# Kernel tuning notes

Measured on AMD Instinct MI355X. Metric: run time of the kernel, lower is better.

## Reference

```python
import jax, jax.numpy as jnp
import numpy as np

B, T, D = 8, 512, 512
MAX_DUR = 15          # durations drawn from [0,16) then clamped to >=1
MAX_LEN = T * MAX_DUR # static padded frame length (torch pads to per-batch max)


def setup_inputs() -> dict:
    key = jax.random.key(0)
    kf, kd = jax.random.split(key)
    features = jax.random.normal(kf, (B, T, D), dtype=jnp.float32)
    durations = jax.random.randint(kd, (B, T), 0, 16, dtype=jnp.int32)
    return {"features": features, "durations": durations}


def reference(features, durations):
    """Duration-based length regulation (variable-length expand + pad).

    For each batch b, phoneme t is repeated durations[b,t] times along the
    frame axis; sequences are zero-padded to MAX_LEN. Implemented as a
    vectorized cumsum + searchsorted gather (no per-element host syncs).
    """
    Bv, Tv, Dv = features.shape
    dur = jnp.maximum(durations, 1)               # clamp(min=1) as in forward()
    cum = jnp.cumsum(dur, axis=1)                 # (B, T) exclusive-right frame boundaries
    pos = jnp.arange(MAX_LEN, dtype=cum.dtype)    # (MAX_LEN,)
    # idx[b, n] = source phoneme for output frame n: count of boundaries <= n
    idx = jax.vmap(lambda c: jnp.searchsorted(c, pos, side="right"))(cum)  # (B, MAX_LEN)
    valid = pos[None, :] < cum[:, -1:]            # (B, MAX_LEN) frames within total length
    idx = jnp.minimum(idx, Tv - 1)                # keep gather in-bounds for padded frames
    out = jnp.take_along_axis(features, idx[..., None], axis=1)  # (B, MAX_LEN, D)
    return jnp.where(valid[..., None], out, jnp.zeros((), features.dtype))
```

## Files before the change

kernel.cpp:

```cpp
#include <hip/hip_runtime.h>

#define BB 8
#define TT 512
#define DD 512
#define MAX_LEN 7680
#define FPB 30
#define HPB (FPB / 2)
#define BPB (MAX_LEN / FPB)

__global__ __launch_bounds__(256) void regulate_kernel(
    const float4* __restrict__ feat,
    const int2*   __restrict__ dur2,
    float4*       __restrict__ out)
{
    __shared__ int ps[256];
    __shared__ int idx_s[FPB];

    const int t    = threadIdx.x;
    const int b    = blockIdx.x / BPB;
    const int base = (blockIdx.x % BPB) * FPB;

    int2 dd = dur2[b * (TT / 2) + t];
    int d0 = dd.x < 1 ? 1 : dd.x;
    int d1 = dd.y < 1 ? 1 : dd.y;
    ps[t] = d0 + d1;

    if (t < FPB) idx_s[t] = -1;
    __syncthreads();

#pragma unroll
    for (int off = 1; off < 256; off <<= 1) {
        int x = (t >= off) ? ps[t - off] : 0;
        __syncthreads();
        ps[t] += x;
        __syncthreads();
    }
    const int incl = ps[t];
    const int s1   = incl - d1;
    const int s0   = s1 - d0;

    const int lim = base + FPB;
    {
        int k0 = s0 > base ? s0 : base;
        int k1 = s1 < lim  ? s1 : lim;
        for (int k = k0; k < k1; ++k) idx_s[k - base] = 2 * t;
        int k2 = s1 > base ? s1 : base;
        int k3 = incl < lim ? incl : lim;
        for (int k = k2; k < k3; ++k) idx_s[k - base] = 2 * t + 1;
    }
    __syncthreads();

    const int lane = t & 127;
    const int sub  = t >> 7;
    const float4* featb = feat + (size_t)b * TT * (DD / 4) + lane;
    float4*       outb  = out  + ((size_t)b * MAX_LEN + base + sub * HPB) * (DD / 4) + lane;

    int    prev = -2;
    float4 val  = make_float4(0.f, 0.f, 0.f, 0.f);
#pragma unroll
    for (int j = 0; j < HPB; ++j) {
        const int src = idx_s[sub * HPB + j];
        if (src != prev) {
            val = (src >= 0) ? featb[(size_t)src * (DD / 4)]
                             : make_float4(0.f, 0.f, 0.f, 0.f);
            prev = src;
        }
        outb[(size_t)j * (DD / 4)] = val;
    }
}

extern "C" void kernel_launch(void* const* d_in, const int* in_sizes, int n_in,
                              void* d_out, int out_size, void* d_ws, size_t ws_size,
                              hipStream_t stream) {
    const float* feat;
    const int*   dur;
    if (in_sizes[0] == BB * TT) {
        dur  = (const int*)d_in[0];
        feat = (const float*)d_in[1];
    } else {
        feat = (const float*)d_in[0];
        dur  = (const int*)d_in[1];
    }
    float* out = (float*)d_out;

    regulate_kernel<<<BB * BPB, 256, 0, stream>>>(
        (const float4*)feat, (const int2*)dur, (float4*)out);
}
```

Before: 138.9 us.

## Replace shared-memory block scan with single-wavefront shuffle scan and larger frame tiles

Each block now computes the duration prefix sum within one 64-lane wavefront: every lane loads and scans eight durations serially, then the lanes combine their totals with shuffle-up. This replaces the 256-thread shared-memory Hillis-Steele scan and its many __syncthreads. Frames per block double from 30 to 60, which halves the number of blocks and so halves the redundant per-block scan work. In exchange each thread writes more output rows, the grid has fewer blocks, and three of the four wavefronts sit idle during the scan.

```diff
diff --git a/kernel.cpp b/kernel.cpp
--- a/kernel.cpp
+++ b/kernel.cpp
@@ -4,62 +4,66 @@
 #define TT 512
 #define DD 512
 #define MAX_LEN 7680
-#define FPB 30
+#define FPB 60
 #define HPB (FPB / 2)
 #define BPB (MAX_LEN / FPB)
 
 __global__ __launch_bounds__(256) void regulate_kernel(
     const float4* __restrict__ feat,
-    const int2*   __restrict__ dur2,
+    const int*    __restrict__ dur,
     float4*       __restrict__ out)
 {
-    __shared__ int ps[256];
     __shared__ int idx_s[FPB];
 
     const int t    = threadIdx.x;
     const int b    = blockIdx.x / BPB;
     const int base = (blockIdx.x % BPB) * FPB;
+    const int lim  = base + FPB;
 
-    int2 dd = dur2[b * (TT / 2) + t];
-    int d0 = dd.x < 1 ? 1 : dd.x;
-    int d1 = dd.y < 1 ? 1 : dd.y;
-    ps[t] = d0 + d1;
+    if (t < 64) {
+        const int l = t;
+        const int4* d4 = (const int4*)(dur + b * TT + 8 * l);
+        int4 a = d4[0], c = d4[1];
+        int d[8] = {a.x, a.y, a.z, a.w, c.x, c.y, c.z, c.w};
+        int s[8];
+        int run = 0;
+#pragma unroll
+        for (int i = 0; i < 8; ++i) {
+            int di = d[i] < 1 ? 1 : d[i];
+            run += di;
+            s[i] = run;
+        }
+        int incl = run;
+#pragma unroll
+        for (int off = 1; off < 64; off <<= 1) {
+            int v = __shfl_up(incl, off, 64);
+            if (l >= off) incl += v;
+        }
+        const int pre = incl - run;
 
-    if (t < FPB) idx_s[t] = -1;
-    __syncthreads();
-
+        for (int j = l; j < FPB; j += 64) idx_s[j] = -1;
 #pragma unroll
-    for (int off = 1; off < 256; off <<= 1) {
-        int x = (t >= off) ? ps[t - off] : 0;
-        __syncthreads();
-        ps[t] += x;
-        __syncthreads();
-    }
-    const int incl = ps[t];
-    const int s1   = incl - d1;
-    const int s0   = s1 - d0;
-
-    const int lim = base + FPB;
-    {
-        int k0 = s0 > base ? s0 : base;
-        int k1 = s1 < lim  ? s1 : lim;
-        for (int k = k0; k < k1; ++k) idx_s[k - base] = 2 * t;
-        int k2 = s1 > base ? s1 : base;
-        int k3 = incl < lim ? incl : lim;
-        for (int k = k2; k < k3; ++k) idx_s[k - base] = 2 * t + 1;
+        for (int i = 0; i < 8; ++i) {
+            int st = pre + (i ? s[i - 1] : 0);
+            int en = pre + s[i];
+            st = st > base ? st : base;
+            en = en < lim ? en : lim;
+            for (int k = st; k < en; ++k) idx_s[k - base] = 8 * l + i;
+        }
     }
     __syncthreads();
 
     const int lane = t & 127;
     const int sub  = t >> 7;
+    const int off  = sub * HPB;
     const float4* featb = feat + (size_t)b * TT * (DD / 4) + lane;
-    float4*       outb  = out  + ((size_t)b * MAX_LEN + base + sub * HPB) * (DD / 4) + lane;
+    float4*       outb  = out  + ((size_t)b * MAX_LEN + base + off) * (DD / 4) + lane;
 
     int    prev = -2;
     float4 val  = make_float4(0.f, 0.f, 0.f, 0.f);
 #pragma unroll
     for (int j = 0; j < HPB; ++j) {
-        const int src = idx_s[sub * HPB + j];
+        const int src = idx_s[off + j];
         if (src != prev) {
             val = (src >= 0) ? featb[(size_t)src * (DD / 4)]
                              : make_float4(0.f, 0.f, 0.f, 0.f);
@@ -84,5 +88,5 @@
     float* out = (float*)d_out;
 
     regulate_kernel<<<BB * BPB, 256, 0, stream>>>(
-        (const float4*)feat, (const int2*)dur, (float4*)out);
+        (const float4*)feat, dur, (float4*)out);
 }
```

After: 141.0 us. About the same (+1.5%).
